# Performance work log

Measured on AMD Instinct MI355X. Metric: run time of the kernel, lower is better.

Reference implementation:

```python
import jax, jax.numpy as jnp
import numpy as np

B, N_PER, E_PER = 100, 1000, 12000  # graphs, nodes/graph, edges/graph
N, E = B * N_PER, B * E_PER
K = int(np.ceil(0.8 * N_PER))  # TopKPooling ratio=0.8 -> 800 kept nodes/graph


def setup_inputs() -> dict:
    key = jax.random.key(0)
    ks = jax.random.split(key, 16)
    g = jnp.repeat(jnp.arange(B, dtype=jnp.int64), E_PER)
    src = g * N_PER + jax.random.randint(ks[0], (E,), 0, N_PER)
    dst = g * N_PER + jax.random.randint(ks[1], (E,), 0, N_PER)
    edge_index = jnp.stack([src, dst]).astype(jnp.int64)
    edge_attr = jax.random.uniform(ks[2], (E,), dtype=jnp.float32) + 0.1  # positive edge weights
    x = jax.random.normal(ks[3], (N, 3), dtype=jnp.float32)
    batch = jnp.repeat(jnp.arange(B, dtype=jnp.int64), N_PER)
    s = 0.1
    return {
        'x': x, 'edge_index': edge_index, 'edge_attr': edge_attr, 'batch': batch,
        'conv1_w': jax.random.normal(ks[4], (3, 64), dtype=jnp.float32) * s,
        'conv1_b': jnp.zeros((64,), dtype=jnp.float32),
        'conv2_w': jax.random.normal(ks[5], (64, 64), dtype=jnp.float32) * s,
        'conv2_b': jnp.zeros((64,), dtype=jnp.float32),
        'pool_w': jax.random.normal(ks[6], (64,), dtype=jnp.float32) * s,
        'lin1_w': jax.random.normal(ks[7], (64, 64), dtype=jnp.float32) * s,
        'lin1_b': jnp.zeros((64,), dtype=jnp.float32),
        'lin2_w': jax.random.normal(ks[8], (64, 32), dtype=jnp.float32) * s,
        'lin2_b': jnp.zeros((32,), dtype=jnp.float32),
        'lin3_w': jax.random.normal(ks[9], (32, 1), dtype=jnp.float32) * s,
        'lin3_b': jnp.zeros((1,), dtype=jnp.float32),
    }


def gcn_conv(x, row, col, ew, W, b):
    # PyG GCNConv with edge_weight and implicit self-loops (weight 1):
    # deg[i] = sum_{e: col=i} ew[e] + 1;  norm_e = d^{-1/2}[row]*ew*d^{-1/2}[col]
    h = x @ W  # [N, out]
    deg = jax.ops.segment_sum(ew, col, num_segments=N) + 1.0
    dinv = jax.lax.rsqrt(deg)
    msg = (dinv[row] * ew * dinv[col])[:, None] * h[row]  # [E, out]
    out = jax.ops.segment_sum(msg, col, num_segments=N)
    out = out + (dinv * dinv)[:, None] * h  # self-loop term
    return out + b


def reference(x, edge_index, edge_attr, batch, conv1_w, conv1_b, conv2_w, conv2_b,
              pool_w, lin1_w, lin1_b, lin2_w, lin2_b, lin3_w, lin3_b):
    row, col = edge_index[0], edge_index[1]
    h = jax.nn.relu(gcn_conv(x, row, col, edge_attr, conv1_w, conv1_b))
    x1 = h.reshape(B, N_PER, 64).mean(axis=1)  # global_mean_pool (equal-size graphs)
    h = jax.nn.relu(gcn_conv(h, row, col, edge_attr, conv2_w, conv2_b))
    # TopKPooling: score = tanh(x.w / ||w||), keep top-K per graph, gate by score
    score = jnp.tanh(h @ pool_w / jnp.linalg.norm(pool_w))  # [N]
    score_bn = score.reshape(B, N_PER)
    vals, idx = jax.lax.top_k(score_bn, K)  # [B, K]
    h_bn = h.reshape(B, N_PER, 64)
    h_sel = jnp.take_along_axis(h_bn, idx[..., None], axis=1) * vals[..., None]
    x2 = h_sel.mean(axis=1)  # global_mean_pool on pooled graph
    z = x1 + x2
    z = jax.nn.relu(z @ lin1_w + lin1_b)
    z = jax.nn.relu(z @ lin2_w + lin2_b)  # dropout is identity in eval mode
    out = jax.nn.sigmoid(z @ lin3_w + lin3_b)[:, 0]
    return out
```

## Files before the change

### kernel.cpp

```cpp
#include <hip/hip_runtime.h>

#define B_G   100
#define N_PER 1000
#define E_PER 12000
#define NTOT  (B_G * N_PER)
#define ETOT  (B_G * E_PER)
#define KSEL  800
#define EPT   12

#define CSRB   0u
#define ENDB   4915200u
#define H2B    5324800u
#define KEYB   11878400u
#define X1BB   12697600u
#define P3NEED 12723200u
#define DLB    12723200u
#define ZB     13132800u
#define SREDB  19532800u
#define P2NEED 19942400u

typedef __attribute__((ext_vector_type(8))) short short8;
typedef __attribute__((ext_vector_type(4))) float float4_;

__device__ __forceinline__ unsigned short f2bf(float f) {
    unsigned u = __float_as_uint(f);
    u += 0x7fffu + ((u >> 16) & 1u);
    return (unsigned short)(u >> 16);
}
__device__ __forceinline__ float upk(unsigned q) {
    return __uint_as_float(q & 0xFFFF0000u);
}
__device__ __forceinline__ float dec_raw(unsigned byte7f) {
    return __uint_as_float(byte7f << 20);
}
__device__ __forceinline__ unsigned enc_fp8(float z) {
    unsigned u = __float_as_uint(z * 0x1p-120f);
    u += 0x7FFFFu + ((u >> 20) & 1u);
    return u >> 20;
}

#define BUILD_BODY(PRE) do {                                                   \
    int esrc[EPT], edst[EPT]; float eww[EPT];                                  \
    int ne = (tid < (E_PER - (EPT - 1) * 1024)) ? EPT : EPT - 1;               \
    _Pragma("unroll")                                                          \
    for (int i = 0; i < EPT; i++) {                                            \
        if (i < ne) {                                                          \
            int e = tid + i * 1024;                                            \
            esrc[i] = ei[ebase + e] - gbase;                                   \
            edst[i] = ei[ETOT + ebase + e] - gbase;                            \
            eww[i]  = ew[ebase + e];                                           \
        }                                                                      \
    }                                                                          \
    ends[tid] = 0;                                                             \
    PRE                                                                        \
    __syncthreads();                                                           \
    _Pragma("unroll")                                                          \
    for (int i = 0; i < EPT; i++)                                              \
        if (i < ne) atomicAdd(&ends[edst[i]], 1);                              \
    __syncthreads();                                                           \
    int v = ends[tid];                                                         \
    int sc = v;                                                                \
    _Pragma("unroll")                                                          \
    for (int m = 1; m < 64; m <<= 1) {                                         \
        int t = __shfl_up(sc, m);                                              \
        if (lane >= m) sc += t;                                                \
    }                                                                          \
    if (lane == 63) wpart[wid] = sc;                                           \
    __syncthreads();                                                           \
    if (tid < 16) {                                                            \
        int s2 = wpart[tid];                                                   \
        _Pragma("unroll")                                                      \
        for (int m = 1; m < 16; m <<= 1) {                                     \
            int t = __shfl_up(s2, m);                                          \
            if (tid >= m) s2 += t;                                             \
        }                                                                      \
        wpart[tid] = s2;                                                       \
    }                                                                          \
    __syncthreads();                                                           \
    int incl = sc + (wid > 0 ? wpart[wid - 1] : 0);                            \
    ends[tid] = incl;                                                          \
    posc[tid] = incl - v;                                                      \
    __syncthreads();                                                           \
    _Pragma("unroll")                                                          \
    for (int i = 0; i < EPT; i++)                                              \
        if (i < ne) {                                                          \
            int p = atomicAdd(&posc[edst[i]], 1);                              \
            csr[p] = ((unsigned)f2bf(eww[i]) << 16) | (unsigned)esrc[i];       \
        }                                                                      \
    __syncthreads();                                                           \
} while (0)

#define WSUM_BODY() do {                                                       \
    if (tid < N_PER) {                                                         \
        int s0i = tid ? ends[tid - 1] : 0;                                     \
        int e0i = ends[tid];                                                   \
        float s0 = 0.f, s1 = 0.f;                                              \
        int k = s0i;                                                           \
        for (; k + 2 <= e0i; k += 2) { s0 += upk(csr[k]); s1 += upk(csr[k + 1]); } \
        if (k < e0i) s0 += upk(csr[k]);                                        \
        float dmy = rsqrtf(s0 + s1 + 1.0f);                                    \
        dl[tid] = dmy;                                                         \
        xl[tid * 3 + 0] *= dmy;                                                \
        xl[tid * 3 + 1] *= dmy;                                                \
        xl[tid * 3 + 2] *= dmy;                                                \
        WSUM_EXTRA                                                             \
    }                                                                          \
    __syncthreads();                                                           \
} while (0)

#define CONV1_NODE(NODE) do {                                                  \
    int node_ = (NODE);                                                        \
    int s0_ = node_ ? ends[node_ - 1] : 0;                                     \
    int e0_ = ends[node_];                                                     \
    float dm_ = dl[node_];                                                     \
    float a0 = xl[node_ * 3 + 0], a1 = xl[node_ * 3 + 1], a2 = xl[node_ * 3 + 2]; \
    for (int k = s0_; k < e0_; k++) {                                          \
        unsigned q = csr[k];                                                   \
        int i0 = (int)(q & 0xFFFFu) * 3;                                       \
        float wv = upk(q);                                                     \
        a0 += wv * xl[i0]; a1 += wv * xl[i0 + 1]; a2 += wv * xl[i0 + 2];       \
    }                                                                          \
    aggv[node_ * 3 + 0] = dm_ * a0;                                            \
    aggv[node_ * 3 + 1] = dm_ * a1;                                            \
    aggv[node_ * 3 + 2] = dm_ * a2;                                            \
} while (0)

#define W1_WAVE(OW, PXSTORE) do {                                              \
    int ow_ = (OW);                                                            \
    float w0 = w1[lane], w1v = w1[64 + lane], w2v = w1[128 + lane], bf = b1[lane]; \
    float px = 0.f;                                                            \
    int chunk = (lane & 31) >> 3;                                              \
    int word  = ((lane >= 32) ? 2 : 0) + ((lane & 7) >> 2);                    \
    for (int node = ow_; node < N_PER; node += 16) {                           \
        float a0 = aggv[node * 3], a1 = aggv[node * 3 + 1], a2 = aggv[node * 3 + 2]; \
        float hv = fmaxf(a0 * w0 + a1 * w1v + a2 * w2v + bf, 0.f);             \
        px += hv;                                                              \
        unsigned byte = enc_fp8(dl[node] * hv);                                \
        unsigned t1 = __shfl_xor(byte, 1);                                     \
        unsigned v16 = (lane & 1) ? (t1 | (byte << 8)) : (byte | (t1 << 8));   \
        unsigned t2 = __shfl_xor(v16, 2);                                      \
        unsigned v32 = (lane & 2) ? (t2 | (v16 << 16)) : (v16 | (t2 << 16));   \
        if ((lane & 3) == 0) {                                                 \
            int cs = chunk ^ ((node >> 1) & 3);                                \
            *(unsigned*)(zs + node * 64 + cs * 16 + word * 4) = v32;           \
        }                                                                      \
    }                                                                          \
    PXSTORE                                                                    \
} while (0)

#define CONV2_TI(TI, AF0, AF1) do {                                            \
    const int t_ = wid + (TI) * 16;                                            \
    const int li_ = t_ * 16 + nloc;                                            \
    const bool valid_ = li_ < N_PER;                                           \
    float acc_[16];                                                            \
    int s_ = 0, cn_ = 0;                                                       \
    if (valid_) {                                                              \
        uint4 rv_ = *(const uint4*)(zs + li_ * 64 + ((kgrp ^ ((li_ >> 1) & 3)) << 4)); \
        _Pragma("unroll")                                                      \
        for (int j = 0; j < 4; j++) {                                          \
            acc_[j]      = dec_raw((rv_.x >> (8 * j)) & 0x7Fu);                \
            acc_[4 + j]  = dec_raw((rv_.y >> (8 * j)) & 0x7Fu);                \
            acc_[8 + j]  = dec_raw((rv_.z >> (8 * j)) & 0x7Fu);                \
            acc_[12 + j] = dec_raw((rv_.w >> (8 * j)) & 0x7Fu);                \
        }                                                                      \
        s_ = li_ ? ends[li_ - 1] : 0;                                          \
        cn_ = ends[li_] - s_;                                                  \
    } else {                                                                   \
        _Pragma("unroll")                                                      \
        for (int j = 0; j < 16; j++) acc_[j] = 0.f;                            \
    }                                                                          \
    int mx_ = cn_;                                                             \
    _Pragma("unroll")                                                          \
    for (int m = 1; m < 16; m <<= 1) mx_ = max(mx_, __shfl_xor(mx_, m));       \
    for (int k = 0; k < mx_; k++) {                                            \
        if (k < cn_) {                                                         \
            unsigned q_ = csr[s_ + k];                                         \
            int src_ = (int)(q_ & 0xFFFFu);                                    \
            float wv_ = upk(q_);                                               \
            uint4 rv_ = *(const uint4*)(zs + src_ * 64 + ((kgrp ^ ((src_ >> 1) & 3)) << 4)); \
            _Pragma("unroll")                                                  \
            for (int j = 0; j < 4; j++) {                                      \
                acc_[j]      += wv_ * dec_raw((rv_.x >> (8 * j)) & 0x7Fu);     \
                acc_[4 + j]  += wv_ * dec_raw((rv_.y >> (8 * j)) & 0x7Fu);     \
                acc_[8 + j]  += wv_ * dec_raw((rv_.z >> (8 * j)) & 0x7Fu);     \
                acc_[12 + j] += wv_ * dec_raw((rv_.w >> (8 * j)) & 0x7Fu);     \
            }                                                                  \
        }                                                                      \
    }                                                                          \
    float scale_ = (valid_ ? dl[li_] : 0.f) * 0x1p120f;                        \
    _Pragma("unroll")                                                          \
    for (int j = 0; j < 8; j++) {                                              \
        AF0[j] = (short)f2bf(scale_ * acc_[j]);                                \
        AF1[j] = (short)f2bf(scale_ * acc_[8 + j]);                            \
    }                                                                          \
} while (0)

#define W2_TI(TI, AF0, AF1, KEYS) do {                                         \
    const int t_ = wid + (TI) * 16;                                            \
    if (t_ < 63) {                                                             \
        float4_ accv_[4];                                                      \
        _Pragma("unroll")                                                      \
        for (int c = 0; c < 4; ++c) accv_[c] = (float4_){0.f, 0.f, 0.f, 0.f};  \
        _Pragma("unroll")                                                      \
        for (int c = 0; c < 4; ++c) {                                          \
            accv_[c] = __builtin_amdgcn_mfma_f32_16x16x32_bf16(AF0, Bf[0][c], accv_[c], 0, 0, 0); \
            accv_[c] = __builtin_amdgcn_mfma_f32_16x16x32_bf16(AF1, Bf[1][c], accv_[c], 0, 0, 0); \
        }                                                                      \
        _Pragma("unroll")                                                      \
        for (int r2 = 0; r2 < 4; ++r2) {                                       \
            int li2_ = t_ * 16 + kgrp * 4 + r2;                                \
            bool valid2_ = li2_ < N_PER;                                       \
            float sp_ = 0.f;                                                   \
            _Pragma("unroll")                                                  \
            for (int c = 0; c < 4; ++c) {                                      \
                float hv_ = fmaxf(accv_[c][r2] + b2c[c], 0.f);                 \
                sp_ += hv_ * pwc[c];                                           \
                if (valid2_) zs[li2_ * 64 + c * 16 + nloc] = (unsigned char)enc_fp8(hv_); \
            }                                                                  \
            _Pragma("unroll")                                                  \
            for (int m = 1; m < 16; m <<= 1) sp_ += __shfl_xor(sp_, m);        \
            if (valid2_ && nloc == 0) {                                        \
                float scv_ = tanhf(sp_ * invn);                                \
                unsigned bits_ = __float_as_uint(scv_);                        \
                unsigned u_ = (bits_ & 0x80000000u) ? ~bits_ : (bits_ | 0x80000000u); \
                (KEYS)[li2_] = ((unsigned long long)u_ << 32) | (unsigned)(1023 - li2_); \
            }                                                                  \
        }                                                                      \
    }                                                                          \
} while (0)

#define W2_SETUP() do {                                                        \
    _Pragma("unroll")                                                          \
    for (int kh = 0; kh < 2; ++kh)                                             \
        _Pragma("unroll")                                                      \
        for (int c = 0; c < 4; ++c) {                                          \
            short8 t;                                                          \
            _Pragma("unroll")                                                  \
            for (int j = 0; j < 8; ++j)                                        \
                t[j] = (short)f2bf(w2[(kh * 32 + kgrp * 8 + j) * 64 + c * 16 + nloc]); \
            Bf[kh][c] = t;                                                     \
        }                                                                      \
    _Pragma("unroll")                                                          \
    for (int c = 0; c < 4; ++c) {                                              \
        b2c[c] = b2[c * 16 + nloc];                                            \
        pwc[c] = pw[c * 16 + nloc];                                            \
    }                                                                          \
    {                                                                          \
        float p = pw[lane], pn = p * p;                                        \
        _Pragma("unroll")                                                      \
        for (int m = 32; m; m >>= 1) pn += __shfl_xor(pn, m);                  \
        invn = rsqrtf(pn);                                                     \
    }                                                                          \
} while (0)

#define TAIL_BODY(OUTIDX) do {                                                 \
    {                                                                          \
        unsigned long long key = keys[tid];                                    \
        for (int k = 2; k <= 1024; k <<= 1) {                                  \
            for (int j = k >> 1; j > 0; j >>= 1) {                             \
                bool desc = (tid & k) == 0;                                    \
                unsigned long long p;                                          \
                if (j >= 64) {                                                 \
                    keys[tid] = key;                                           \
                    __syncthreads();                                           \
                    p = keys[tid ^ j];                                         \
                    __syncthreads();                                           \
                } else {                                                       \
                    p = __shfl_xor(key, j);                                    \
                }                                                              \
                bool low = (tid & j) == 0;                                     \
                bool sw = low ? (desc ? (key < p) : (key > p))                 \
                              : (desc ? (p < key) : (p > key));                \
                if (sw) key = p;                                               \
            }                                                                  \
        }                                                                      \
        keys[tid] = key;                                                       \
    }                                                                          \
    __syncthreads();                                                           \
    {                                                                          \
        int f = tid & 63, w16 = tid >> 6;                                      \
        float acc2 = 0.f;                                                      \
        for (int r = w16; r < KSEL; r += 16) {                                 \
            unsigned long long key = keys[r];                                  \
            int idx = 1023 - (int)(key & 0xFFFFFFFFu);                         \
            unsigned u = (unsigned)(key >> 32);                                \
            unsigned bits = (u & 0x80000000u) ? (u & 0x7FFFFFFFu) : ~u;        \
            float valS = __uint_as_float(bits) * 0x1p120f;                     \
            acc2 += valS * dec_raw((unsigned)zs[idx * 64 + f] & 0x7Fu);        \
        }                                                                      \
        red[tid] = acc2;                                                       \
    }                                                                          \
    __syncthreads();                                                           \
    if (tid < 64) {                                                            \
        float s2 = 0.f;                                                        \
        for (int ww = 0; ww < 16; ww++) s2 += red[ww * 64 + tid];              \
        zbuf[tid] = x1b[tid] + s2 * (1.0f / KSEL);                             \
    }                                                                          \
    __syncthreads();                                                           \
    if (tid < 64) {                                                            \
        float a = l1b[tid];                                                    \
        for (int k = 0; k < 64; k++) a += zbuf[k] * l1w[k * 64 + tid];         \
        a1buf[tid] = fmaxf(a, 0.f);                                            \
    }                                                                          \
    __syncthreads();                                                           \
    if (tid < 32) {                                                            \
        float a = l2b[tid];                                                    \
        for (int k = 0; k < 64; k++) a += a1buf[k] * l2w[k * 32 + tid];        \
        a2buf[tid] = fmaxf(a, 0.f);                                            \
    }                                                                          \
    __syncthreads();                                                           \
    if (tid == 0) {                                                            \
        float t = l3b[0];                                                      \
        for (int k = 0; k < 32; k++) t += a2buf[k] * l3w[k];                   \
        out[OUTIDX] = 1.0f / (1.0f + expf(-t));                                \
    }                                                                          \
} while (0)

#define SMEM_DECLS()                                                           \
    __shared__ __align__(16) unsigned char smem[136832];                       \
    unsigned char* zs = smem;                                                  \
    float* xl = (float*)smem;                                                  \
    unsigned* csr = (unsigned*)(smem + 64000);                                 \
    int*   ends = (int*)(smem + 112000);                                       \
    float* dl   = (float*)(smem + 116096);                                     \
    int*   posc = (int*)(smem + 116096);                                       \
    int*   wpart = (int*)(smem + 120192);                                      \
    float* x1b   = (float*)(smem + 120192);                                    \
    unsigned char* uA = smem + 120448;                                         \
    float* aggv = (float*)uA;                                                  \
    (void)posc; (void)wpart; (void)aggv; (void)x1b; (void)zs;

__global__ __launch_bounds__(1024) void k_build(
    const int* __restrict__ ei, const float* __restrict__ ew,
    unsigned char* __restrict__ ws) {
    __shared__ __align__(16) unsigned csr[12000];
    __shared__ int ends[1024];
    __shared__ int posc[1024];
    __shared__ int wpart[16];
    int g = blockIdx.x, tid = threadIdx.x;
    int wid = tid >> 6, lane = tid & 63;
    int gbase = g * N_PER, ebase = g * E_PER;
    BUILD_BODY();
    {
        uint4* cw = (uint4*)(ws + CSRB + (size_t)g * 49152);
        const uint4* cs = (const uint4*)csr;
        for (int i = tid; i < 3000; i += 1024) cw[i] = cs[i];
        ((int*)(ws + ENDB + (size_t)g * 4096))[tid] = ends[tid];
    }
}

#define WSUM_EXTRA if (h == 0) dlws[tid] = dmy;
__global__ __launch_bounds__(1024)
__attribute__((amdgpu_waves_per_eu(4, 4))) void k_front2(
    const float* __restrict__ x,
    const float* __restrict__ w1, const float* __restrict__ b1,
    unsigned char* __restrict__ ws) {
    SMEM_DECLS();
    int g = blockIdx.x >> 1, h = blockIdx.x & 1, tid = threadIdx.x;
    int wid = tid >> 6, lane = tid & 63;
    int gbase = g * N_PER;
    float* dlws = (float*)(ws + DLB + (size_t)g * 4096);
    {
        const uint4* cs = (const uint4*)(ws + CSRB + (size_t)g * 49152);
        uint4* cd = (uint4*)csr;
        for (int i = tid; i < 3000; i += 1024) cd[i] = cs[i];
        ends[tid] = ((const int*)(ws + ENDB + (size_t)g * 4096))[tid];
        for (int i = tid; i < N_PER * 3; i += 1024) xl[i] = x[(size_t)gbase * 3 + i];
    }
    __syncthreads();
    WSUM_BODY();
    if (tid < 500) CONV1_NODE(2 * tid + h);
    __syncthreads();
    if (wid < 8)
        W1_WAVE(h + 2 * wid,
                { ((float*)(ws + SREDB + (size_t)g * 4096))[ow_ * 64 + lane] = px; });
    __syncthreads();
    {
        uint4* zw = (uint4*)(ws + ZB + (size_t)g * 64000);
        const uint4* zv = (const uint4*)zs;
        for (int i = tid; i < 4000; i += 1024)
            if (((i >> 2) & 1) == h) zw[i] = zv[i];
    }
}
#undef WSUM_EXTRA

__global__ __launch_bounds__(1024)
__attribute__((amdgpu_waves_per_eu(4, 4))) void k_conv2(
    const float* __restrict__ w2, const float* __restrict__ b2,
    const float* __restrict__ pw, unsigned char* __restrict__ ws) {
    SMEM_DECLS();
    int g = blockIdx.x >> 1, h = blockIdx.x & 1, tid = threadIdx.x;
    int wid = tid >> 6, lane = tid & 63;
    unsigned long long* kw = (unsigned long long*)(ws + KEYB + (size_t)g * 8192);
    {
        const uint4* zsrc = (const uint4*)(ws + ZB + (size_t)g * 64000);
        uint4* zd = (uint4*)zs;
        for (int i = tid; i < 4000; i += 1024) zd[i] = zsrc[i];
        const uint4* cs = (const uint4*)(ws + CSRB + (size_t)g * 49152);
        uint4* cd = (uint4*)csr;
        for (int i = tid; i < 3000; i += 1024) cd[i] = cs[i];
        ends[tid] = ((const int*)(ws + ENDB + (size_t)g * 4096))[tid];
        if (tid < N_PER) dl[tid] = ((const float*)(ws + DLB + (size_t)g * 4096))[tid];
    }
    __syncthreads();
    int kgrp = lane >> 4, nloc = lane & 15;
    const int tiA = h * 2, tiB = h * 2 + 1;
    short8 AfAa, AfAb, AfBa, AfBb;
    CONV2_TI(tiA, AfAa, AfAb);
    CONV2_TI(tiB, AfBa, AfBb);
    __syncthreads();
    {
        short8 Bf[2][4]; float b2c[4], pwc[4], invn;
        W2_SETUP();
        if (h == 1 && tid >= N_PER) kw[tid] = 0ull;
        W2_TI(tiA, AfAa, AfAb, kw);
        W2_TI(tiB, AfBa, AfBb, kw);
    }
    __syncthreads();
    {
        uint4* d = (uint4*)(ws + H2B + (size_t)g * 65536);
        const uint4* s = (const uint4*)zs;
        int lo = h * 2048, hi = h ? 4000 : 2048;
        for (int i = lo + tid; i < hi; i += 1024) d[i] = s[i];
    }
}

#define WSUM_EXTRA
__global__ __launch_bounds__(1024)
__attribute__((amdgpu_waves_per_eu(4, 4))) void k_mid(
    const float* __restrict__ x,
    const float* __restrict__ w1, const float* __restrict__ b1,
    const float* __restrict__ w2, const float* __restrict__ b2,
    const float* __restrict__ pw, unsigned char* __restrict__ ws) {
    SMEM_DECLS();
    int g = blockIdx.x >> 1, half = blockIdx.x & 1, tid = threadIdx.x;
    int wid = tid >> 6, lane = tid & 63;
    int gbase = g * N_PER;
    {
        const uint4* cs = (const uint4*)(ws + CSRB + (size_t)g * 49152);
        uint4* cd = (uint4*)csr;
        for (int i = tid; i < 3000; i += 1024) cd[i] = cs[i];
        ends[tid] = ((const int*)(ws + ENDB + (size_t)g * 4096))[tid];
        for (int i = tid; i < N_PER * 3; i += 1024) xl[i] = x[(size_t)gbase * 3 + i];
    }
    __syncthreads();
    WSUM_BODY();
    if (tid < N_PER) CONV1_NODE(tid);
    __syncthreads();
    {
        float* sred = (float*)(uA + 12288);
        if (wid < 16) W1_WAVE(wid, { sred[ow_ * 64 + lane] = px; });
        __syncthreads();
        if (tid < 64) {
            float t = 0.f;
            for (int r = 0; r < 16; r++) t += sred[r * 64 + tid];
            x1b[tid] = t * (1.0f / N_PER);
        }
    }
    int kgrp = lane >> 4, nloc = lane & 15;
    const int tiA = half * 2, tiB = half * 2 + 1;
    short8 AfAa, AfAb, AfBa, AfBb;
    CONV2_TI(tiA, AfAa, AfAb);
    CONV2_TI(tiB, AfBa, AfBb);
    __syncthreads();
    unsigned long long* keys = (unsigned long long*)uA;
    {
        short8 Bf[2][4]; float b2c[4], pwc[4], invn;
        W2_SETUP();
        if (tid >= N_PER) keys[tid] = 0ull;
        W2_TI(tiA, AfAa, AfAb, keys);
        W2_TI(tiB, AfBa, AfBb, keys);
    }
    __syncthreads();
    {
        uint4* d = (uint4*)(ws + H2B + (size_t)g * 65536 + (size_t)half * 32768);
        const uint4* s = (const uint4*)(zs + half * 32768);
        int n = half ? 1952 : 2048;
        for (int i = tid; i < n; i += 1024) d[i] = s[i];
        unsigned long long* kw2 =
            (unsigned long long*)(ws + KEYB + (size_t)g * 8192);
        for (int i = tid; i < 512; i += 1024)
            kw2[half * 512 + i] = keys[half * 512 + i];
        if (!half && tid < 64)
            ((float*)(ws + X1BB + (size_t)g * 256))[tid] = x1b[tid];
    }
}
#undef WSUM_EXTRA

__global__ __launch_bounds__(1024) void k_tail(
    const float* __restrict__ l1w, const float* __restrict__ l1b,
    const float* __restrict__ l2w, const float* __restrict__ l2b,
    const float* __restrict__ l3w, const float* __restrict__ l3b,
    float* __restrict__ out, const unsigned char* __restrict__ ws, int mode) {
    __shared__ __align__(16) unsigned char sm2[77184];
    unsigned char* zs = sm2;
    unsigned long long* keys = (unsigned long long*)(sm2 + 64000);
    float* red   = (float*)(sm2 + 72192);
    float* x1b   = (float*)(sm2 + 76288);
    float* a1buf = (float*)(sm2 + 76544);
    float* a2buf = (float*)(sm2 + 76800);
    float* zbuf  = (float*)(sm2 + 76928);
    int g = blockIdx.x, tid = threadIdx.x;
    {
        uint4* hd = (uint4*)zs;
        const uint4* hs = (const uint4*)(ws + H2B + (size_t)g * 65536);
        for (int i = tid; i < 4000; i += 1024) hd[i] = hs[i];
        keys[tid] = ((const unsigned long long*)(ws + KEYB + (size_t)g * 8192))[tid];
        if (tid < 64) {
            if (mode) {
                const float* sr = (const float*)(ws + SREDB + (size_t)g * 4096);
                float t = 0.f;
                for (int r = 0; r < 16; r++) t += sr[r * 64 + tid];
                x1b[tid] = t * (1.0f / N_PER);
            } else {
                x1b[tid] = ((const float*)(ws + X1BB + (size_t)g * 256))[tid];
            }
        }
    }
    __syncthreads();
    TAIL_BODY(g);
}

#define WSUM_EXTRA
__global__ __launch_bounds__(1024)
__attribute__((amdgpu_waves_per_eu(4, 4))) void k_all_single(
    const int* __restrict__ ei, const float* __restrict__ ew,
    const float* __restrict__ x,
    const float* __restrict__ w1, const float* __restrict__ b1,
    const float* __restrict__ w2, const float* __restrict__ b2,
    const float* __restrict__ pw,
    const float* __restrict__ l1w, const float* __restrict__ l1b,
    const float* __restrict__ l2w, const float* __restrict__ l2b,
    const float* __restrict__ l3w, const float* __restrict__ l3b,
    float* __restrict__ out) {
    SMEM_DECLS();
    int g = blockIdx.x, tid = threadIdx.x;
    int wid = tid >> 6, lane = tid & 63;
    int gbase = g * N_PER, ebase = g * E_PER;
    BUILD_BODY(for (int i = tid; i < N_PER * 3; i += 1024) xl[i] = x[(size_t)gbase * 3 + i];);
    WSUM_BODY();
    if (tid < N_PER) CONV1_NODE(tid);
    __syncthreads();
    {
        float* sred = (float*)(uA + 12288);
        if (wid < 16) W1_WAVE(wid, { sred[ow_ * 64 + lane] = px; });
        __syncthreads();
        if (tid < 64) {
            float t = 0.f;
            for (int r = 0; r < 16; r++) t += sred[r * 64 + tid];
            x1b[tid] = t * (1.0f / N_PER);
        }
    }
    int kgrp = lane >> 4, nloc = lane & 15;
    short8 Af0a, Af0b, Af1a, Af1b, Af2a, Af2b, Af3a, Af3b;
    CONV2_TI(0, Af0a, Af0b);
    CONV2_TI(1, Af1a, Af1b);
    CONV2_TI(2, Af2a, Af2b);
    CONV2_TI(3, Af3a, Af3b);
    __syncthreads();
    unsigned long long* keys = (unsigned long long*)uA;
    {
        short8 Bf[2][4]; float b2c[4], pwc[4], invn;
        W2_SETUP();
        if (tid >= N_PER) keys[tid] = 0ull;
        W2_TI(0, Af0a, Af0b, keys);
        W2_TI(1, Af1a, Af1b, keys);
        W2_TI(2, Af2a, Af2b, keys);
        W2_TI(3, Af3a, Af3b, keys);
    }
    __syncthreads();
    float* red   = (float*)(uA + 8192);
    float* a1buf = (float*)(uA + 12288);
    float* a2buf = (float*)(uA + 12544);
    float* zbuf  = (float*)(uA + 12672);
    TAIL_BODY(g);
}
#undef WSUM_EXTRA

extern "C" void kernel_launch(void* const* d_in, const int* in_sizes, int n_in,
                              void* d_out, int out_size, void* d_ws, size_t ws_size,
                              hipStream_t stream) {
    const float* x   = (const float*)d_in[0];
    const int*   ei  = (const int*)d_in[1];
    const float* ew  = (const float*)d_in[2];
    const float* c1w = (const float*)d_in[4];
    const float* c1b = (const float*)d_in[5];
    const float* c2w = (const float*)d_in[6];
    const float* c2b = (const float*)d_in[7];
    const float* pw  = (const float*)d_in[8];
    const float* l1w = (const float*)d_in[9];
    const float* l1b = (const float*)d_in[10];
    const float* l2w = (const float*)d_in[11];
    const float* l2b = (const float*)d_in[12];
    const float* l3w = (const float*)d_in[13];
    const float* l3b = (const float*)d_in[14];
    float* out = (float*)d_out;
    (void)in_sizes; (void)n_in; (void)out_size;

    unsigned char* ws = (unsigned char*)d_ws;
    if (d_ws != nullptr && ws_size >= (size_t)P2NEED) {
        k_build<<<B_G, 1024, 0, stream>>>(ei, ew, ws);
        k_front2<<<2 * B_G, 1024, 0, stream>>>(x, c1w, c1b, ws);
        k_conv2<<<2 * B_G, 1024, 0, stream>>>(c2w, c2b, pw, ws);
        k_tail<<<B_G, 1024, 0, stream>>>(l1w, l1b, l2w, l2b, l3w, l3b, out, ws, 1);
    } else if (d_ws != nullptr && ws_size >= (size_t)P3NEED) {
        k_build<<<B_G, 1024, 0, stream>>>(ei, ew, ws);
        k_mid<<<2 * B_G, 1024, 0, stream>>>(x, c1w, c1b, c2w, c2b, pw, ws);
        k_tail<<<B_G, 1024, 0, stream>>>(l1w, l1b, l2w, l2b, l3w, l3b, out, ws, 0);
    } else {
        k_all_single<<<B_G, 1024, 0, stream>>>(
            ei, ew, x, c1w, c1b, c2w, c2b, pw,
            l1w, l1b, l2w, l2b, l3w, l3b, out);
    }
}
```

Measured before the change: 174.9 us.

## Fuse four-kernel pipeline into one paired-block kernel with flag-based handoff

Replaces the build/front/conv2/tail kernel sequence with a single kernel in which two blocks per graph each rebuild the CSR locally and cooperate via global-memory release/acquire flags. Partial conv1 and conv2 results and top-k keys are exchanged through workspace, and one block finishes the tail. This removes three kernel launch boundaries and the CSR round trip through global memory. In exchange the CSR build is done twice per graph, a memset launch is added to clear the flags, and spin-waiting relies on both blocks of a pair being co-resident; the spin has a cap rather than a guarantee.

```diff
diff --git a/kernel.cpp b/kernel.cpp
--- a/kernel.cpp
+++ b/kernel.cpp
@@ -8,16 +8,15 @@
 #define KSEL  800
 #define EPT   12
 
-#define CSRB   0u
-#define ENDB   4915200u
-#define H2B    5324800u
-#define KEYB   11878400u
-#define X1BB   12697600u
-#define P3NEED 12723200u
-#define DLB    12723200u
-#define ZB     13132800u
-#define SREDB  19532800u
-#define P2NEED 19942400u
+#define FLAG1B 0u
+#define FLAG2B 1024u
+#define ZXB    4096u
+#define SREDXB 6404096u
+#define H2XB   6813696u
+#define KEYXB  10090496u
+#define WSNEED 10500096u
+
+#define SPINCAP 200000
 
 typedef __attribute__((ext_vector_type(8))) short short8;
 typedef __attribute__((ext_vector_type(4))) float float4_;
@@ -103,7 +102,6 @@
         xl[tid * 3 + 0] *= dmy;                                                \
         xl[tid * 3 + 1] *= dmy;                                                \
         xl[tid * 3 + 2] *= dmy;                                                \
-        WSUM_EXTRA                                                             \
     }                                                                          \
     __syncthreads();                                                           \
 } while (0)
@@ -330,135 +328,65 @@
     float* aggv = (float*)uA;                                                  \
     (void)posc; (void)wpart; (void)aggv; (void)x1b; (void)zs;
 
-__global__ __launch_bounds__(1024) void k_build(
+__global__ __launch_bounds__(1024)
+__attribute__((amdgpu_waves_per_eu(4, 4))) void k_pair2(
     const int* __restrict__ ei, const float* __restrict__ ew,
-    unsigned char* __restrict__ ws) {
-    __shared__ __align__(16) unsigned csr[12000];
-    __shared__ int ends[1024];
-    __shared__ int posc[1024];
-    __shared__ int wpart[16];
-    int g = blockIdx.x, tid = threadIdx.x;
-    int wid = tid >> 6, lane = tid & 63;
-    int gbase = g * N_PER, ebase = g * E_PER;
-    BUILD_BODY();
-    {
-        uint4* cw = (uint4*)(ws + CSRB + (size_t)g * 49152);
-        const uint4* cs = (const uint4*)csr;
-        for (int i = tid; i < 3000; i += 1024) cw[i] = cs[i];
-        ((int*)(ws + ENDB + (size_t)g * 4096))[tid] = ends[tid];
-    }
-}
-
-#define WSUM_EXTRA if (h == 0) dlws[tid] = dmy;
-__global__ __launch_bounds__(1024)
-__attribute__((amdgpu_waves_per_eu(4, 4))) void k_front2(
     const float* __restrict__ x,
     const float* __restrict__ w1, const float* __restrict__ b1,
-    unsigned char* __restrict__ ws) {
+    const float* __restrict__ w2, const float* __restrict__ b2,
+    const float* __restrict__ pw,
+    const float* __restrict__ l1w, const float* __restrict__ l1b,
+    const float* __restrict__ l2w, const float* __restrict__ l2b,
+    const float* __restrict__ l3w, const float* __restrict__ l3b,
+    float* __restrict__ out, unsigned char* __restrict__ ws) {
     SMEM_DECLS();
     int g = blockIdx.x >> 1, h = blockIdx.x & 1, tid = threadIdx.x;
     int wid = tid >> 6, lane = tid & 63;
-    int gbase = g * N_PER;
-    float* dlws = (float*)(ws + DLB + (size_t)g * 4096);
-    {
-        const uint4* cs = (const uint4*)(ws + CSRB + (size_t)g * 49152);
-        uint4* cd = (uint4*)csr;
-        for (int i = tid; i < 3000; i += 1024) cd[i] = cs[i];
-        ends[tid] = ((const int*)(ws + ENDB + (size_t)g * 4096))[tid];
-        for (int i = tid; i < N_PER * 3; i += 1024) xl[i] = x[(size_t)gbase * 3 + i];
-    }
-    __syncthreads();
+    int gbase = g * N_PER, ebase = g * E_PER;
+    unsigned* flag1 = (unsigned*)(ws + FLAG1B);
+    unsigned* flag2 = (unsigned*)(ws + FLAG2B);
+    unsigned char* zx = ws + ZXB + (size_t)g * 64000;
+    float* sredx = (float*)(ws + SREDXB + (size_t)g * 4096);
+    unsigned char* h2x = ws + H2XB + (size_t)g * 32768;
+    unsigned long long* kx = (unsigned long long*)(ws + KEYXB + (size_t)g * 4096);
+
+    BUILD_BODY(for (int i = tid; i < N_PER * 3; i += 1024) xl[i] = x[(size_t)gbase * 3 + i];);
     WSUM_BODY();
     if (tid < 500) CONV1_NODE(2 * tid + h);
     __syncthreads();
     if (wid < 8)
-        W1_WAVE(h + 2 * wid,
-                { ((float*)(ws + SREDB + (size_t)g * 4096))[ow_ * 64 + lane] = px; });
+        W1_WAVE(2 * wid + h, { sredx[ow_ * 64 + lane] = px; });
     __syncthreads();
     {
-        uint4* zw = (uint4*)(ws + ZB + (size_t)g * 64000);
+        uint4* zw = (uint4*)zx;
         const uint4* zv = (const uint4*)zs;
         for (int i = tid; i < 4000; i += 1024)
             if (((i >> 2) & 1) == h) zw[i] = zv[i];
     }
-}
-#undef WSUM_EXTRA
-
-__global__ __launch_bounds__(1024)
-__attribute__((amdgpu_waves_per_eu(4, 4))) void k_conv2(
-    const float* __restrict__ w2, const float* __restrict__ b2,
-    const float* __restrict__ pw, unsigned char* __restrict__ ws) {
-    SMEM_DECLS();
-    int g = blockIdx.x >> 1, h = blockIdx.x & 1, tid = threadIdx.x;
-    int wid = tid >> 6, lane = tid & 63;
-    unsigned long long* kw = (unsigned long long*)(ws + KEYB + (size_t)g * 8192);
+    __syncthreads();
+    if (tid == 0)
+        __hip_atomic_store(&flag1[g * 2 + h], 1u, __ATOMIC_RELEASE,
+                           __HIP_MEMORY_SCOPE_AGENT);
+    if (tid == 0) {
+        for (int it = 0; it < SPINCAP; ++it) {
+            if (__hip_atomic_load(&flag1[g * 2 + (1 - h)], __ATOMIC_ACQUIRE,
+                                  __HIP_MEMORY_SCOPE_AGENT) != 0u) break;
+            __builtin_amdgcn_s_sleep(8);
+        }
+    }
+    __syncthreads();
     {
-        const uint4* zsrc = (const uint4*)(ws + ZB + (size_t)g * 64000);
+        unsigned f1 = __hip_atomic_load(&flag1[g * 2 + (1 - h)], __ATOMIC_ACQUIRE,
+                                        __HIP_MEMORY_SCOPE_AGENT);
+        asm volatile("" :: "s"(f1));
+        const uint4* zr = (const uint4*)zx;
         uint4* zd = (uint4*)zs;
-        for (int i = tid; i < 4000; i += 1024) zd[i] = zsrc[i];
-        const uint4* cs = (const uint4*)(ws + CSRB + (size_t)g * 49152);
-        uint4* cd = (uint4*)csr;
-        for (int i = tid; i < 3000; i += 1024) cd[i] = cs[i];
-        ends[tid] = ((const int*)(ws + ENDB + (size_t)g * 4096))[tid];
-        if (tid < N_PER) dl[tid] = ((const float*)(ws + DLB + (size_t)g * 4096))[tid];
+        for (int i = tid; i < 4000; i += 1024)
+            if (((i >> 2) & 1) == (1 - h)) zd[i] = zr[i];
     }
     __syncthreads();
     int kgrp = lane >> 4, nloc = lane & 15;
     const int tiA = h * 2, tiB = h * 2 + 1;
-    short8 AfAa, AfAb, AfBa, AfBb;
-    CONV2_TI(tiA, AfAa, AfAb);
-    CONV2_TI(tiB, AfBa, AfBb);
-    __syncthreads();
-    {
-        short8 Bf[2][4]; float b2c[4], pwc[4], invn;
-        W2_SETUP();
-        if (h == 1 && tid >= N_PER) kw[tid] = 0ull;
-        W2_TI(tiA, AfAa, AfAb, kw);
-        W2_TI(tiB, AfBa, AfBb, kw);
-    }
-    __syncthreads();
-    {
-        uint4* d = (uint4*)(ws + H2B + (size_t)g * 65536);
-        const uint4* s = (const uint4*)zs;
-        int lo = h * 2048, hi = h ? 4000 : 2048;
-        for (int i = lo + tid; i < hi; i += 1024) d[i] = s[i];
-    }
-}
-
-#define WSUM_EXTRA
-__global__ __launch_bounds__(1024)
-__attribute__((amdgpu_waves_per_eu(4, 4))) void k_mid(
-    const float* __restrict__ x,
-    const float* __restrict__ w1, const float* __restrict__ b1,
-    const float* __restrict__ w2, const float* __restrict__ b2,
-    const float* __restrict__ pw, unsigned char* __restrict__ ws) {
-    SMEM_DECLS();
-    int g = blockIdx.x >> 1, half = blockIdx.x & 1, tid = threadIdx.x;
-    int wid = tid >> 6, lane = tid & 63;
-    int gbase = g * N_PER;
-    {
-        const uint4* cs = (const uint4*)(ws + CSRB + (size_t)g * 49152);
-        uint4* cd = (uint4*)csr;
-        for (int i = tid; i < 3000; i += 1024) cd[i] = cs[i];
-        ends[tid] = ((const int*)(ws + ENDB + (size_t)g * 4096))[tid];
-        for (int i = tid; i < N_PER * 3; i += 1024) xl[i] = x[(size_t)gbase * 3 + i];
-    }
-    __syncthreads();
-    WSUM_BODY();
-    if (tid < N_PER) CONV1_NODE(tid);
-    __syncthreads();
-    {
-        float* sred = (float*)(uA + 12288);
-        if (wid < 16) W1_WAVE(wid, { sred[ow_ * 64 + lane] = px; });
-        __syncthreads();
-        if (tid < 64) {
-            float t = 0.f;
-            for (int r = 0; r < 16; r++) t += sred[r * 64 + tid];
-            x1b[tid] = t * (1.0f / N_PER);
-        }
-    }
-    int kgrp = lane >> 4, nloc = lane & 15;
-    const int tiA = half * 2, tiB = half * 2 + 1;
     short8 AfAa, AfAb, AfBa, AfBb;
     CONV2_TI(tiA, AfAa, AfAb);
     CONV2_TI(tiB, AfBa, AfBb);
@@ -472,56 +400,47 @@
         W2_TI(tiB, AfBa, AfBb, keys);
     }
     __syncthreads();
+    if (h) {
+        const uint4* srcv = (const uint4*)(zs + 32768);
+        uint4* dstv = (uint4*)h2x;
+        for (int i = tid; i < 1952; i += 1024) dstv[i] = srcv[i];
+        for (int i = tid; i < 512; i += 1024) kx[i] = keys[512 + i];
+        __syncthreads();
+        if (tid == 0)
+            __hip_atomic_store(&flag2[g], 1u, __ATOMIC_RELEASE,
+                               __HIP_MEMORY_SCOPE_AGENT);
+        return;
+    }
+    if (tid == 0) {
+        for (int it = 0; it < SPINCAP; ++it) {
+            if (__hip_atomic_load(&flag2[g], __ATOMIC_ACQUIRE,
+                                  __HIP_MEMORY_SCOPE_AGENT) != 0u) break;
+            __builtin_amdgcn_s_sleep(8);
+        }
+    }
+    __syncthreads();
     {
-        uint4* d = (uint4*)(ws + H2B + (size_t)g * 65536 + (size_t)half * 32768);
-        const uint4* s = (const uint4*)(zs + half * 32768);
-        int n = half ? 1952 : 2048;
-        for (int i = tid; i < n; i += 1024) d[i] = s[i];
-        unsigned long long* kw2 =
-            (unsigned long long*)(ws + KEYB + (size_t)g * 8192);
-        for (int i = tid; i < 512; i += 1024)
-            kw2[half * 512 + i] = keys[half * 512 + i];
-        if (!half && tid < 64)
-            ((float*)(ws + X1BB + (size_t)g * 256))[tid] = x1b[tid];
-    }
-}
-#undef WSUM_EXTRA
-
-__global__ __launch_bounds__(1024) void k_tail(
-    const float* __restrict__ l1w, const float* __restrict__ l1b,
-    const float* __restrict__ l2w, const float* __restrict__ l2b,
-    const float* __restrict__ l3w, const float* __restrict__ l3b,
-    float* __restrict__ out, const unsigned char* __restrict__ ws, int mode) {
-    __shared__ __align__(16) unsigned char sm2[77184];
-    unsigned char* zs = sm2;
-    unsigned long long* keys = (unsigned long long*)(sm2 + 64000);
-    float* red   = (float*)(sm2 + 72192);
-    float* x1b   = (float*)(sm2 + 76288);
-    float* a1buf = (float*)(sm2 + 76544);
-    float* a2buf = (float*)(sm2 + 76800);
-    float* zbuf  = (float*)(sm2 + 76928);
-    int g = blockIdx.x, tid = threadIdx.x;
-    {
-        uint4* hd = (uint4*)zs;
-        const uint4* hs = (const uint4*)(ws + H2B + (size_t)g * 65536);
-        for (int i = tid; i < 4000; i += 1024) hd[i] = hs[i];
-        keys[tid] = ((const unsigned long long*)(ws + KEYB + (size_t)g * 8192))[tid];
+        unsigned f2 = __hip_atomic_load(&flag2[g], __ATOMIC_ACQUIRE,
+                                        __HIP_MEMORY_SCOPE_AGENT);
+        asm volatile("" :: "s"(f2));
+        uint4* dstv = (uint4*)(zs + 32768);
+        const uint4* srcv = (const uint4*)h2x;
+        for (int i = tid; i < 1952; i += 1024) dstv[i] = srcv[i];
+        for (int i = tid; i < 512; i += 1024) keys[512 + i] = kx[i];
         if (tid < 64) {
-            if (mode) {
-                const float* sr = (const float*)(ws + SREDB + (size_t)g * 4096);
-                float t = 0.f;
-                for (int r = 0; r < 16; r++) t += sr[r * 64 + tid];
-                x1b[tid] = t * (1.0f / N_PER);
-            } else {
-                x1b[tid] = ((const float*)(ws + X1BB + (size_t)g * 256))[tid];
-            }
+            float t = 0.f;
+            for (int r = 0; r < 16; r++) t += sredx[r * 64 + tid];
+            x1b[tid] = t * (1.0f / N_PER);
         }
     }
     __syncthreads();
+    float* red   = (float*)(uA + 8192);
+    float* a1buf = (float*)(uA + 12288);
+    float* a2buf = (float*)(uA + 12544);
+    float* zbuf  = (float*)(uA + 12672);
     TAIL_BODY(g);
 }
 
-#define WSUM_EXTRA
 __global__ __launch_bounds__(1024)
 __attribute__((amdgpu_waves_per_eu(4, 4))) void k_all_single(
     const int* __restrict__ ei, const float* __restrict__ ew,
@@ -575,7 +494,6 @@
     float* zbuf  = (float*)(uA + 12672);
     TAIL_BODY(g);
 }
-#undef WSUM_EXTRA
 
 extern "C" void kernel_launch(void* const* d_in, const int* in_sizes, int n_in,
                               void* d_out, int out_size, void* d_ws, size_t ws_size,
@@ -597,16 +515,11 @@
     float* out = (float*)d_out;
     (void)in_sizes; (void)n_in; (void)out_size;
 
-    unsigned char* ws = (unsigned char*)d_ws;
-    if (d_ws != nullptr && ws_size >= (size_t)P2NEED) {
-        k_build<<<B_G, 1024, 0, stream>>>(ei, ew, ws);
-        k_front2<<<2 * B_G, 1024, 0, stream>>>(x, c1w, c1b, ws);
-        k_conv2<<<2 * B_G, 1024, 0, stream>>>(c2w, c2b, pw, ws);
-        k_tail<<<B_G, 1024, 0, stream>>>(l1w, l1b, l2w, l2b, l3w, l3b, out, ws, 1);
-    } else if (d_ws != nullptr && ws_size >= (size_t)P3NEED) {
-        k_build<<<B_G, 1024, 0, stream>>>(ei, ew, ws);
-        k_mid<<<2 * B_G, 1024, 0, stream>>>(x, c1w, c1b, c2w, c2b, pw, ws);
-        k_tail<<<B_G, 1024, 0, stream>>>(l1w, l1b, l2w, l2b, l3w, l3b, out, ws, 0);
+    if (d_ws != nullptr && ws_size >= (size_t)WSNEED) {
+        hipMemsetAsync(d_ws, 0, 4096, stream);
+        k_pair2<<<2 * B_G, 1024, 0, stream>>>(
+            ei, ew, x, c1w, c1b, c2w, c2b, pw,
+            l1w, l1b, l2w, l2b, l3w, l3b, out, (unsigned char*)d_ws);
     } else {
         k_all_single<<<B_G, 1024, 0, stream>>>(
             ei, ew, x, c1w, c1b, c2w, c2b, pw,
```

Result: slower. 222.4 us (+27.1%).
